# Kernel tuning notes

Hardware: AMD Instinct MI355X
Metric: run time of the kernel (lower is better)

Reference implementation:

```python
import jax, jax.numpy as jnp
import numpy as np
import math

B, S, D, H, W = 1, 2048, 512, 8, 64
DK = D // H
NEG = -1e9


def setup_inputs() -> dict:
    rng = jax.random.key(0)
    ks = jax.random.split(rng, 8)
    sc = 0.02
    return {
        "query": jax.random.normal(ks[0], (B, S, D), jnp.float32),
        "key": jax.random.normal(ks[1], (B, S, D), jnp.float32),
        "value": jax.random.normal(ks[2], (B, S, D), jnp.float32),
        "Wq": jax.random.normal(ks[3], (D, D), jnp.float32) * sc,
        "Wk": jax.random.normal(ks[4], (D, D), jnp.float32) * sc,
        "Wv": jax.random.normal(ks[5], (D, D), jnp.float32) * sc,
        "Wo": jax.random.normal(ks[6], (D, D), jnp.float32) * sc,
        "bo": jax.random.normal(ks[7], (D,), jnp.float32) * sc,
    }


def reference(query, key, value, Wq, Wk, Wv, Wo, bo):
    b, s, d = query.shape

    def proj(x, Wm):
        # [B,S,D] -> [B,H,S,DK]
        return (x @ Wm.T).reshape(b, s, H, DK).transpose(0, 2, 1, 3)

    Q = proj(query, Wq)
    K = proj(key, Wk)
    V = proj(value, Wv)

    i = jnp.arange(s)
    rel = jnp.arange(-W, 1)                     # causal band: keys i-W..i
    idx = i[:, None] + rel[None, :]             # [S, W+1]
    valid = idx >= 0
    idxc = jnp.clip(idx, 0, s - 1)

    Kw = K[:, :, idxc, :]                       # [B,H,S,W+1,DK]
    Vw = V[:, :, idxc, :]

    scores = jnp.einsum('bhsd,bhsrd->bhsr', Q, Kw) / math.sqrt(DK)
    decay_bias = 0.1 * jnp.exp(-0.1 * jnp.abs(rel.astype(jnp.float32)))
    scores = jnp.where(valid[None, None], scores + decay_bias, NEG)
    probs = jax.nn.softmax(scores, axis=-1)     # [B,H,S,W+1]

    out = jnp.einsum('bhsr,bhsrd->bhsd', probs, Vw)
    out = out.transpose(0, 2, 1, 3).reshape(b, s, d)
    output = out @ Wo.T + bo

    # attention_weights [B,H,S,2W]: only rows with window_size <= 2W are written
    win = jnp.minimum(s, i + W + 1) - jnp.maximum(0, i - W)   # [S]
    stored = win <= 2 * W
    slot = jnp.arange(2 * W)
    ridx = slot[None, :] + jnp.maximum(W - i, 0)[:, None]     # [S,2W] slot->band index
    vmask = (ridx <= W) & (slot[None, :] < win[:, None]) & stored[:, None]
    gath = jnp.take_along_axis(probs, jnp.clip(ridx, 0, W)[None, None], axis=-1)
    attn_w = jnp.where(vmask[None, None], gath, 0.0)

    return output, attn_w
```

## Files before the change

kernel.cpp:

```cpp
#include <hip/hip_runtime.h>
#include <stdint.h>

#define SEQ   2048
#define DM    512
#define NHEAD 8
#define DKH   64
#define WIN   64
#define NEGV  -1000000000.0f

typedef __attribute__((ext_vector_type(8))) short          short8;
typedef __attribute__((ext_vector_type(4))) float          float4v;
typedef __attribute__((ext_vector_type(8))) unsigned short ushort8v;

__device__ __forceinline__ unsigned short f2bf(float x) {
    uint32_t u = __float_as_uint(x);
    uint32_t r = (u + 0x7FFFu + ((u >> 16) & 1u)) >> 16;
    return (unsigned short)r;
}
__device__ __forceinline__ float bf2f(unsigned short u) {
    return __uint_as_float(((uint32_t)u) << 16);
}

__device__ __forceinline__ void async_cp16(const void* g, void* lds) {
    __builtin_amdgcn_global_load_lds(
        (const __attribute__((address_space(1))) unsigned int*)(uintptr_t)g,
        (__attribute__((address_space(3))) unsigned int*)(uint32_t)(uintptr_t)lds,
        16, 0, 0);
}

__global__ __launch_bounds__(256)
void cast7_kernel(const float* __restrict__ q, const float* __restrict__ k,
                  const float* __restrict__ v, const float* __restrict__ wq,
                  const float* __restrict__ wk, const float* __restrict__ wv,
                  const float* __restrict__ wo, unsigned short* __restrict__ dst)
{
    int g = (blockIdx.x * 256 + threadIdx.x) * 8;
    const float* src; int off;
    if      (g < 1048576) { src = q;  off = g; }
    else if (g < 2097152) { src = k;  off = g - 1048576; }
    else if (g < 3145728) { src = v;  off = g - 2097152; }
    else if (g < 3407872) { src = wq; off = g - 3145728; }
    else if (g < 3670016) { src = wk; off = g - 3407872; }
    else if (g < 3932160) { src = wv; off = g - 3670016; }
    else                  { src = wo; off = g - 3932160; }
    float4 x0 = *(const float4*)(src + off);
    float4 x1 = *(const float4*)(src + off + 4);
    ushort8v o;
    o[0] = f2bf(x0.x); o[1] = f2bf(x0.y); o[2] = f2bf(x0.z); o[3] = f2bf(x0.w);
    o[4] = f2bf(x1.x); o[5] = f2bf(x1.y); o[6] = f2bf(x1.z); o[7] = f2bf(x1.w);
    *(ushort8v*)(dst + g) = o;
}

template<bool BIAS, bool OUT_BF16>
__device__ __forceinline__ void gemm_mfma_body(const unsigned short* __restrict__ A,
                                               const unsigned short* __restrict__ B,
                                               const float* __restrict__ bias,
                                               void* __restrict__ Cv)
{
    __shared__ __align__(16) unsigned short As[128 * 32];
    __shared__ __align__(16) unsigned short Bs[128 * 32];

    const int tid  = threadIdx.x;
    const int m0   = blockIdx.x * 128;
    const int n0   = blockIdx.y * 128;
    const int lane = tid & 63;
    const int wave = tid >> 6;
    const int wm   = (wave >> 1) * 64;
    const int wn   = (wave & 1) * 64;
    const int lm   = lane & 15;
    const int lk   = (lane >> 4) * 8;

    float4v acc[4][4] = {};

    for (int k0 = 0; k0 < 512; k0 += 32) {
        #pragma unroll
        for (int h = 0; h < 2; h++) {
            int c  = tid + h * 256;
            int r  = c >> 2;
            int kc = (c & 3) * 8;
            async_cp16(A + (size_t)(m0 + r) * 512 + k0 + kc, As + c * 8);
            async_cp16(B + (size_t)(n0 + r) * 512 + k0 + kc, Bs + c * 8);
        }
        __syncthreads();

        short8 av[4], bv[4];
        #pragma unroll
        for (int mt = 0; mt < 4; mt++)
            av[mt] = *(const short8*)(As + (wm + mt * 16 + lm) * 32 + lk);
        #pragma unroll
        for (int nt = 0; nt < 4; nt++)
            bv[nt] = *(const short8*)(Bs + (wn + nt * 16 + lm) * 32 + lk);
        #pragma unroll
        for (int mt = 0; mt < 4; mt++)
            #pragma unroll
            for (int nt = 0; nt < 4; nt++)
                acc[mt][nt] = __builtin_amdgcn_mfma_f32_16x16x32_bf16(
                    av[mt], bv[nt], acc[mt][nt], 0, 0, 0);
        __syncthreads();
    }

    const int r0 = (lane >> 4) * 4;
    const int cn = lane & 15;
    #pragma unroll
    for (int nt = 0; nt < 4; nt++) {
        int gcol = n0 + wn + nt * 16 + cn;
        float b = BIAS ? bias[gcol] : 0.f;
        #pragma unroll
        for (int mt = 0; mt < 4; mt++) {
            int grow = m0 + wm + mt * 16 + r0;
            #pragma unroll
            for (int reg = 0; reg < 4; reg++) {
                float val = acc[mt][nt][reg] + b;
                if (OUT_BF16)
                    ((unsigned short*)Cv)[(size_t)(grow + reg) * 512 + gcol] = f2bf(val);
                else
                    ((float*)Cv)[(size_t)(grow + reg) * 512 + gcol] = val;
            }
        }
    }
}

__global__ __launch_bounds__(256)
void qkv_gemm_kernel(const unsigned short* __restrict__ qb,
                     const unsigned short* __restrict__ kb,
                     const unsigned short* __restrict__ vb,
                     const unsigned short* __restrict__ wqb,
                     const unsigned short* __restrict__ wkb,
                     const unsigned short* __restrict__ wvb,
                     unsigned short* __restrict__ Qp, unsigned short* __restrict__ Kp,
                     unsigned short* __restrict__ Vp)
{
    const unsigned short *A, *B; unsigned short* C;
    if (blockIdx.z == 0)      { A = qb; B = wqb; C = Qp; }
    else if (blockIdx.z == 1) { A = kb; B = wkb; C = Kp; }
    else                      { A = vb; B = wvb; C = Vp; }
    gemm_mfma_body<false, true>(A, B, nullptr, C);
}

__global__ __launch_bounds__(256)
void out_gemm_kernel(const unsigned short* __restrict__ ctxb,
                     const unsigned short* __restrict__ wob,
                     const float* __restrict__ bo, float* __restrict__ out)
{
    gemm_mfma_body<true, false>(ctxb, wob, bo, out);
}

#define VTS 152

__global__ __launch_bounds__(256)
void attn_kernel(const unsigned short* __restrict__ Qp,
                 const unsigned short* __restrict__ Kp,
                 const unsigned short* __restrict__ Vp,
                 unsigned short* __restrict__ ctxb,
                 float* __restrict__ attnw)
{
    __shared__ __align__(16) unsigned short Qs[64 * 72];
    __shared__ __align__(16) unsigned short Ks[128 * 72];
    __shared__ __align__(16) unsigned short Vt[64 * VTS];
    __shared__ __align__(16) unsigned short Ps[4][16][96];

    const int h   = blockIdx.y;
    const int q0  = blockIdx.x * 64;
    const int tid = threadIdx.x;

    for (int c = tid; c < 512; c += 256) {
        int row = c >> 3, ch = c & 7;
        *(ushort8v*)&Qs[row * 72 + ch * 8] =
            *(const ushort8v*)&Qp[(size_t)(q0 + row) * 512 + h * 64 + ch * 8];
    }
    for (int c = tid; c < 1024; c += 256) {
        int row = c >> 3, ch = c & 7;
        int g = q0 - 64 + row;
        ushort8v val = {0, 0, 0, 0, 0, 0, 0, 0};
        if (g >= 0)
            val = *(const ushort8v*)&Kp[(size_t)g * 512 + h * 64 + ch * 8];
        *(ushort8v*)&Ks[row * 72 + ch * 8] = val;
    }
    {
        int key = tid >> 1, dh = tid & 1;
        int g = q0 - 64 + key;
        ushort8v vv[4];
        #pragma unroll
        for (int j = 0; j < 4; j++) {
            ushort8v z = {0, 0, 0, 0, 0, 0, 0, 0};
            vv[j] = (g >= 0)
                ? *(const ushort8v*)&Vp[(size_t)g * 512 + h * 64 + dh * 32 + j * 8]
                : z;
        }
        #pragma unroll
        for (int j = 0; j < 4; j++)
            #pragma unroll
            for (int e = 0; e < 8; e++)
                Vt[(dh * 32 + j * 8 + e) * VTS + key] = vv[j][e];
    }
    for (int t = tid; t < 64 * 24; t += 256) {
        int d = t / 24, c = 128 + (t % 24);
        Vt[d * VTS + c] = 0;
    }
    __syncthreads();

    const int lane = tid & 63;
    const int w    = tid >> 6;
    const int lm   = lane & 15;
    const int g16  = lane >> 4;
    const int lk8  = g16 * 8;

    short8 av0 = *(const short8*)&Qs[(w * 16 + lm) * 72 + lk8];
    short8 av1 = *(const short8*)&Qs[(w * 16 + lm) * 72 + 32 + lk8];
    float4v sc[5];
    #pragma unroll
    for (int kt = 0; kt < 5; kt++) {
        const unsigned short* kr = &Ks[(w * 16 + kt * 16 + lm) * 72];
        short8 b0 = *(const short8*)(kr + lk8);
        short8 b1 = *(const short8*)(kr + 32 + lk8);
        float4v a = {0.f, 0.f, 0.f, 0.f};
        a = __builtin_amdgcn_mfma_f32_16x16x32_bf16(av0, b0, a, 0, 0, 0);
        a = __builtin_amdgcn_mfma_f32_16x16x32_bf16(av1, b1, a, 0, 0, 0);
        sc[kt] = a;
    }

    float v[5][4];
    #pragma unroll
    for (int kt = 0; kt < 5; kt++) {
        int kk = kt * 16 + lm;
        int g  = q0 - 64 + w * 16 + kk;
        #pragma unroll
        for (int reg = 0; reg < 4; reg++) {
            int rr = g16 * 4 + reg;
            bool valid = (kk >= rr) && (kk <= rr + 64) && (g >= 0);
            v[kt][reg] = valid
                ? sc[kt][reg] * 0.125f + 0.1f * __expf(-0.1f * (float)(64 + rr - kk))
                : NEGV;
        }
    }

    float mx[4], sm[4];
    #pragma unroll
    for (int reg = 0; reg < 4; reg++) {
        float m = v[0][reg];
        #pragma unroll
        for (int kt = 1; kt < 5; kt++) m = fmaxf(m, v[kt][reg]);
        mx[reg] = m;
    }
    #pragma unroll
    for (int off = 1; off < 16; off <<= 1)
        #pragma unroll
        for (int reg = 0; reg < 4; reg++)
            mx[reg] = fmaxf(mx[reg], __shfl_xor(mx[reg], off));
    float p[5][4];
    #pragma unroll
    for (int reg = 0; reg < 4; reg++) {
        float s = 0.f;
        #pragma unroll
        for (int kt = 0; kt < 5; kt++) {
            float e = __expf(v[kt][reg] - mx[reg]);
            p[kt][reg] = e;
            s += e;
        }
        sm[reg] = s;
    }
    #pragma unroll
    for (int off = 1; off < 16; off <<= 1)
        #pragma unroll
        for (int reg = 0; reg < 4; reg++)
            sm[reg] += __shfl_xor(sm[reg], off);
    #pragma unroll
    for (int reg = 0; reg < 4; reg++) {
        float inv = 1.f / sm[reg];
        #pragma unroll
        for (int kt = 0; kt < 5; kt++) p[kt][reg] *= inv;
    }

    #pragma unroll
    for (int kt = 0; kt < 5; kt++)
        #pragma unroll
        for (int reg = 0; reg < 4; reg++)
            Ps[w][g16 * 4 + reg][kt * 16 + lm] = f2bf(p[kt][reg]);
    #pragma unroll
    for (int reg = 0; reg < 4; reg++)
        Ps[w][g16 * 4 + reg][80 + lm] = 0;

    __syncthreads();

    float4v oacc[4] = {};
    #pragma unroll
    for (int ks = 0; ks < 3; ks++) {
        short8 pa = *(const short8*)&Ps[w][lm][ks * 32 + lk8];
        #pragma unroll
        for (int nt = 0; nt < 4; nt++) {
            short8 vb = *(const short8*)&Vt[(nt * 16 + lm) * VTS + w * 16 + ks * 32 + lk8];
            oacc[nt] = __builtin_amdgcn_mfma_f32_16x16x32_bf16(pa, vb, oacc[nt], 0, 0, 0);
        }
    }

    #pragma unroll
    for (int nt = 0; nt < 4; nt++)
        #pragma unroll
        for (int reg = 0; reg < 4; reg++) {
            int i = q0 + w * 16 + g16 * 4 + reg;
            ctxb[(size_t)i * 512 + h * 64 + nt * 16 + lm] = f2bf(oacc[nt][reg]);
        }

    __syncthreads();

    for (int t = tid; t < 64 * 128; t += 256) {
        int ql = t >> 7, slot = t & 127;
        int i  = q0 + ql;
        float val = 0.f;
        if (q0 == 0) {
            if (slot <= ql) {
                int kk = (ql & 15) + slot + 64 - ql;
                val = bf2f(Ps[ql >> 4][ql & 15][kk]);
            }
        } else if (q0 == SEQ - 64) {
            if (slot <= 64) {
                int kk = (ql & 15) + slot;
                val = bf2f(Ps[ql >> 4][ql & 15][kk]);
            }
        }
        attnw[((size_t)h * SEQ + i) * 2 * WIN + slot] = val;
    }
}

extern "C" void kernel_launch(void* const* d_in, const int* in_sizes, int n_in,
                              void* d_out, int out_size, void* d_ws, size_t ws_size,
                              hipStream_t stream)
{
    const float* query = (const float*)d_in[0];
    const float* key   = (const float*)d_in[1];
    const float* value = (const float*)d_in[2];
    const float* Wq    = (const float*)d_in[3];
    const float* Wk    = (const float*)d_in[4];
    const float* Wv    = (const float*)d_in[5];
    const float* Wo    = (const float*)d_in[6];
    const float* bo    = (const float*)d_in[7];

    float* out   = (float*)d_out;
    float* attnw = out + SEQ * DM;

    unsigned short* qb   = (unsigned short*)d_ws;
    unsigned short* kb   = qb  + 1048576;
    unsigned short* vb   = kb  + 1048576;
    unsigned short* wqb  = vb  + 1048576;
    unsigned short* wkb  = wqb + 262144;
    unsigned short* wvb  = wkb + 262144;
    unsigned short* wob  = wvb + 262144;
    unsigned short* Qp   = wob + 262144;
    unsigned short* Kp   = Qp  + 1048576;
    unsigned short* Vp   = Kp  + 1048576;
    unsigned short* ctxb = Vp  + 1048576;

    cast7_kernel<<<2048, 256, 0, stream>>>(query, key, value, Wq, Wk, Wv, Wo, qb);

    dim3 g1(SEQ / 128, DM / 128, 3);
    qkv_gemm_kernel<<<g1, 256, 0, stream>>>(qb, kb, vb, wqb, wkb, wvb, Qp, Kp, Vp);

    dim3 g2(SEQ / 64, NHEAD);
    attn_kernel<<<g2, 256, 0, stream>>>(Qp, Kp, Vp, ctxb, attnw);

    dim3 g3(SEQ / 128, DM / 128);
    out_gemm_kernel<<<g3, 256, 0, stream>>>(ctxb, wob, bo, out);
}
```

Before: 112.8 us.

## Fuse fp32-to-bf16 casts into GEMM tile loads and drop cast kernel

Removes the separate cast kernel that converted inputs and weights to bf16 in workspace. The GEMMs now load fp32 directly, convert in registers, and store to LDS, which saves one launch and a full read-write pass over the inputs. The async global-to-LDS copies are replaced by register prefetch of the next K tile, a simple software pipeline. In exchange, each GEMM block reads twice the bytes and repeats conversions, since A and B tiles are loaded by several blocks.

```diff
diff --git a/kernel.cpp b/kernel.cpp
--- a/kernel.cpp
+++ b/kernel.cpp
@@ -21,41 +21,20 @@
     return __uint_as_float(((uint32_t)u) << 16);
 }
 
-__device__ __forceinline__ void async_cp16(const void* g, void* lds) {
-    __builtin_amdgcn_global_load_lds(
-        (const __attribute__((address_space(1))) unsigned int*)(uintptr_t)g,
-        (__attribute__((address_space(3))) unsigned int*)(uint32_t)(uintptr_t)lds,
-        16, 0, 0);
-}
-
-__global__ __launch_bounds__(256)
-void cast7_kernel(const float* __restrict__ q, const float* __restrict__ k,
-                  const float* __restrict__ v, const float* __restrict__ wq,
-                  const float* __restrict__ wk, const float* __restrict__ wv,
-                  const float* __restrict__ wo, unsigned short* __restrict__ dst)
-{
-    int g = (blockIdx.x * 256 + threadIdx.x) * 8;
-    const float* src; int off;
-    if      (g < 1048576) { src = q;  off = g; }
-    else if (g < 2097152) { src = k;  off = g - 1048576; }
-    else if (g < 3145728) { src = v;  off = g - 2097152; }
-    else if (g < 3407872) { src = wq; off = g - 3145728; }
-    else if (g < 3670016) { src = wk; off = g - 3407872; }
-    else if (g < 3932160) { src = wv; off = g - 3670016; }
-    else                  { src = wo; off = g - 3932160; }
-    float4 x0 = *(const float4*)(src + off);
-    float4 x1 = *(const float4*)(src + off + 4);
+__device__ __forceinline__ ushort8v ldcvt8(const float* __restrict__ p) {
+    float4 x0 = *(const float4*)p;
+    float4 x1 = *(const float4*)(p + 4);
     ushort8v o;
     o[0] = f2bf(x0.x); o[1] = f2bf(x0.y); o[2] = f2bf(x0.z); o[3] = f2bf(x0.w);
     o[4] = f2bf(x1.x); o[5] = f2bf(x1.y); o[6] = f2bf(x1.z); o[7] = f2bf(x1.w);
-    *(ushort8v*)(dst + g) = o;
-}
-
-template<bool BIAS, bool OUT_BF16>
-__device__ __forceinline__ void gemm_mfma_body(const unsigned short* __restrict__ A,
-                                               const unsigned short* __restrict__ B,
-                                               const float* __restrict__ bias,
-                                               void* __restrict__ Cv)
+    return o;
+}
+
+template<bool BIAS, bool OUT_BF16, bool A_F32, bool B_F32>
+__device__ __forceinline__ void gemm_body(const void* __restrict__ Ap,
+                                          const void* __restrict__ Bp,
+                                          const float* __restrict__ bias,
+                                          void* __restrict__ Cv)
 {
     __shared__ __align__(16) unsigned short As[128 * 32];
     __shared__ __align__(16) unsigned short Bs[128 * 32];
@@ -69,17 +48,42 @@
     const int wn   = (wave & 1) * 64;
     const int lm   = lane & 15;
     const int lk   = (lane >> 4) * 8;
+    const int r    = tid >> 2;
+    const int kc   = (tid & 3) * 8;
+
+    const float* Af = (const float*)Ap;
+    const unsigned short* Ab = (const unsigned short*)Ap;
+    const float* Bf = (const float*)Bp;
+    const unsigned short* Bb = (const unsigned short*)Bp;
 
     float4v acc[4][4] = {};
 
+    ushort8v a0, a1, b0, b1;
+    if (A_F32) { a0 = ldcvt8(Af + (size_t)(m0 + r) * 512 + kc);
+                 a1 = ldcvt8(Af + (size_t)(m0 + r + 64) * 512 + kc); }
+    else       { a0 = *(const ushort8v*)(Ab + (size_t)(m0 + r) * 512 + kc);
+                 a1 = *(const ushort8v*)(Ab + (size_t)(m0 + r + 64) * 512 + kc); }
+    if (B_F32) { b0 = ldcvt8(Bf + (size_t)(n0 + r) * 512 + kc);
+                 b1 = ldcvt8(Bf + (size_t)(n0 + r + 64) * 512 + kc); }
+    else       { b0 = *(const ushort8v*)(Bb + (size_t)(n0 + r) * 512 + kc);
+                 b1 = *(const ushort8v*)(Bb + (size_t)(n0 + r + 64) * 512 + kc); }
+
     for (int k0 = 0; k0 < 512; k0 += 32) {
-        #pragma unroll
-        for (int h = 0; h < 2; h++) {
-            int c  = tid + h * 256;
-            int r  = c >> 2;
-            int kc = (c & 3) * 8;
-            async_cp16(A + (size_t)(m0 + r) * 512 + k0 + kc, As + c * 8);
-            async_cp16(B + (size_t)(n0 + r) * 512 + k0 + kc, Bs + c * 8);
+        *(ushort8v*)(As + (size_t)tid * 8)         = a0;
+        *(ushort8v*)(As + (size_t)(tid + 256) * 8) = a1;
+        *(ushort8v*)(Bs + (size_t)tid * 8)         = b0;
+        *(ushort8v*)(Bs + (size_t)(tid + 256) * 8) = b1;
+
+        int kn = k0 + 32;
+        if (kn < 512) {
+            if (A_F32) { a0 = ldcvt8(Af + (size_t)(m0 + r) * 512 + kn + kc);
+                         a1 = ldcvt8(Af + (size_t)(m0 + r + 64) * 512 + kn + kc); }
+            else       { a0 = *(const ushort8v*)(Ab + (size_t)(m0 + r) * 512 + kn + kc);
+                         a1 = *(const ushort8v*)(Ab + (size_t)(m0 + r + 64) * 512 + kn + kc); }
+            if (B_F32) { b0 = ldcvt8(Bf + (size_t)(n0 + r) * 512 + kn + kc);
+                         b1 = ldcvt8(Bf + (size_t)(n0 + r + 64) * 512 + kn + kc); }
+            else       { b0 = *(const ushort8v*)(Bb + (size_t)(n0 + r) * 512 + kn + kc);
+                         b1 = *(const ushort8v*)(Bb + (size_t)(n0 + r + 64) * 512 + kn + kc); }
         }
         __syncthreads();
 
@@ -121,28 +125,26 @@
 }
 
 __global__ __launch_bounds__(256)
-void qkv_gemm_kernel(const unsigned short* __restrict__ qb,
-                     const unsigned short* __restrict__ kb,
-                     const unsigned short* __restrict__ vb,
-                     const unsigned short* __restrict__ wqb,
-                     const unsigned short* __restrict__ wkb,
-                     const unsigned short* __restrict__ wvb,
+void qkv_gemm_kernel(const float* __restrict__ q, const float* __restrict__ k,
+                     const float* __restrict__ v,
+                     const float* __restrict__ Wq, const float* __restrict__ Wk,
+                     const float* __restrict__ Wv,
                      unsigned short* __restrict__ Qp, unsigned short* __restrict__ Kp,
                      unsigned short* __restrict__ Vp)
 {
-    const unsigned short *A, *B; unsigned short* C;
-    if (blockIdx.z == 0)      { A = qb; B = wqb; C = Qp; }
-    else if (blockIdx.z == 1) { A = kb; B = wkb; C = Kp; }
-    else                      { A = vb; B = wvb; C = Vp; }
-    gemm_mfma_body<false, true>(A, B, nullptr, C);
+    const float *A, *B; unsigned short* C;
+    if (blockIdx.z == 0)      { A = q; B = Wq; C = Qp; }
+    else if (blockIdx.z == 1) { A = k; B = Wk; C = Kp; }
+    else                      { A = v; B = Wv; C = Vp; }
+    gemm_body<false, true, true, true>(A, B, nullptr, C);
 }
 
 __global__ __launch_bounds__(256)
 void out_gemm_kernel(const unsigned short* __restrict__ ctxb,
-                     const unsigned short* __restrict__ wob,
+                     const float* __restrict__ Wo,
                      const float* __restrict__ bo, float* __restrict__ out)
 {
-    gemm_mfma_body<true, false>(ctxb, wob, bo, out);
+    gemm_body<true, false, false, true>(ctxb, Wo, bo, out);
 }
 
 #define VTS 152
@@ -338,26 +340,18 @@
     float* out   = (float*)d_out;
     float* attnw = out + SEQ * DM;
 
-    unsigned short* qb   = (unsigned short*)d_ws;
-    unsigned short* kb   = qb  + 1048576;
-    unsigned short* vb   = kb  + 1048576;
-    unsigned short* wqb  = vb  + 1048576;
-    unsigned short* wkb  = wqb + 262144;
-    unsigned short* wvb  = wkb + 262144;
-    unsigned short* wob  = wvb + 262144;
-    unsigned short* Qp   = wob + 262144;
-    unsigned short* Kp   = Qp  + 1048576;
-    unsigned short* Vp   = Kp  + 1048576;
-    unsigned short* ctxb = Vp  + 1048576;
-
-    cast7_kernel<<<2048, 256, 0, stream>>>(query, key, value, Wq, Wk, Wv, Wo, qb);
+    unsigned short* Qp   = (unsigned short*)d_ws;
+    unsigned short* Kp   = Qp + 1048576;
+    unsigned short* Vp   = Kp + 1048576;
+    unsigned short* ctxb = Vp + 1048576;
 
     dim3 g1(SEQ / 128, DM / 128, 3);
-    qkv_gemm_kernel<<<g1, 256, 0, stream>>>(qb, kb, vb, wqb, wkb, wvb, Qp, Kp, Vp);
+    qkv_gemm_kernel<<<g1, 256, 0, stream>>>(query, key, value, Wq, Wk, Wv,
+                                            Qp, Kp, Vp);
 
     dim3 g2(SEQ / 64, NHEAD);
     attn_kernel<<<g2, 256, 0, stream>>>(Qp, Kp, Vp, ctxb, attnw);
 
     dim3 g3(SEQ / 128, DM / 128);
-    out_gemm_kernel<<<g3, 256, 0, stream>>>(ctxb, wob, bo, out);
-}
+    out_gemm_kernel<<<g3, 256, 0, stream>>>(ctxb, Wo, bo, out);
+}
```

Result: slower. 120.7 us (+7.0%).
